# Performance work log

Measured on AMD Instinct MI355X. Metric: run time of the kernel, lower is better.

Reference implementation:

```python
import jax, jax.numpy as jnp
import numpy as np
from jax import lax

B, T, I, H = 32, 512, 512, 1024


def setup_inputs() -> dict:
    key = jax.random.key(0)
    k0, k1, k2, k3, k4 = jax.random.split(key, 5)
    s_i = 1.0 / np.sqrt(I).astype(np.float32)
    s_h = 1.0 / np.sqrt(H).astype(np.float32)
    x = jax.random.normal(k0, (B, T, I), dtype=jnp.float32)
    # stacked gate weights, order: input(i), forget(f), cell(g), output(o)
    Wx = jax.random.uniform(k1, (4 * H, I), jnp.float32, -s_i, s_i)
    bx = jax.random.uniform(k2, (4 * H,), jnp.float32, -s_i, s_i)
    Wh = jax.random.uniform(k3, (4 * H, H), jnp.float32, -s_h, s_h)
    bh = jax.random.uniform(k4, (4 * H,), jnp.float32, -s_h, s_h)
    return {"x": x, "Wx": Wx, "bx": bx, "Wh": Wh, "bh": bh}


def reference(x, Wx, bx, Wh, bh):
    # Pre-compute all input-to-gate projections in one batched GEMM: [B,T,4H]
    xg = jnp.einsum("bti,gi->btg", x, Wx) + bx + bh

    def step(carry, xg_t):
        h, c = carry
        gates = xg_t + h @ Wh.T  # [B,4H]
        i, f, g, o = jnp.split(gates, 4, axis=-1)
        i = jax.nn.sigmoid(i)
        f = jax.nn.sigmoid(f)
        g = jnp.tanh(g)
        o = jax.nn.sigmoid(o)
        c = f * c + i * g
        h = o * jnp.tanh(c)  # r is None in forward -> h_tilde = tanh(c)
        return (h, c), h

    b = x.shape[0]
    h0 = jnp.zeros((b, H), dtype=x.dtype)
    c0 = jnp.zeros((b, H), dtype=x.dtype)
    _, hs = lax.scan(step, (h0, c0), jnp.swapaxes(xg, 0, 1))  # hs: [T,B,H]
    return jnp.swapaxes(hs, 0, 1)  # [B,T,H]
```

## Files before the change

### kernel.cpp

```cpp
#include <hip/hip_runtime.h>
#include <hip/hip_bf16.h>

#define Bv 32
#define Tv 512
#define Iv 512
#define Hv 1024
#define NG 4096

typedef short bf16x8 __attribute__((ext_vector_type(8)));
typedef float floatx16 __attribute__((ext_vector_type(16)));
typedef unsigned short u16;
typedef unsigned long long u64;

__device__ __forceinline__ u16 f2bf(float f) {
  __hip_bfloat16 h = __float2bfloat16(f);
  return *reinterpret_cast<u16*>(&h);
}

__device__ __forceinline__ floatx16 mfma32(bf16x8 a, bf16x8 b, floatx16 c) {
  return __builtin_amdgcn_mfma_f32_32x32x16_bf16(a, b, c, 0, 0, 0);
}

__device__ __forceinline__ u64 ld_agent_u64(const u64* p) {
  return __hip_atomic_load(p, __ATOMIC_RELAXED, __HIP_MEMORY_SCOPE_AGENT);
}
__device__ __forceinline__ void st_agent_u16(u16* p, u16 v) {
  __hip_atomic_store(p, v, __ATOMIC_RELAXED, __HIP_MEMORY_SCOPE_AGENT);
}

__device__ __forceinline__ bf16x8 mk_frag(u64 lo, u64 hi) {
  union { u64 q[2]; bf16x8 v; } u;
  u.q[0] = lo; u.q[1] = hi;
  return u.v;
}

__global__ void k_init(unsigned int* p, int n) {
  int i = blockIdx.x * blockDim.x + threadIdx.x;
  if (i < n) p[i] = 0u;
}

__global__ void k_f2bf(const float* __restrict__ in, u16* __restrict__ out, int n) {
  int i = blockIdx.x * blockDim.x + threadIdx.x;
  if (i < n) out[i] = f2bf(in[i]);
}

__global__ void k_whf(const float* __restrict__ Wh, u16* __restrict__ whf) {
  int tid = blockIdx.x * 256 + threadIdx.x;
  int lane = tid & 63;
  int kt   = (tid >> 6) & 63;
  int nt   = (tid >> 12) & 1;
  int bl   = tid >> 13;
  int r    = nt * 32 + (lane & 31);
  int gate = r >> 4, du = r & 15;
  int row  = gate * Hv + bl * 16 + du;
  int k0   = kt * 16 + (lane >> 5) * 8;
  const float* s = Wh + (size_t)row * Hv + k0;
  u16* d = whf + (size_t)tid * 8;
#pragma unroll
  for (int j = 0; j < 8; ++j) d[j] = f2bf(s[j]);
}

__global__ __launch_bounds__(256) void k_xg(const u16* __restrict__ xb, const u16* __restrict__ wxb,
                                            const float* __restrict__ bx, const float* __restrict__ bh,
                                            float* __restrict__ xg, int t0, int tcshift) {
  __shared__ u16 Al[128 * 40];
  __shared__ u16 Bl[128 * 40];
  int tid = threadIdx.x;
  int wave = tid >> 6, lane = tid & 63;
  int wm = wave & 1, wn = wave >> 1;
  int bm = blockIdx.x, bn = blockIdx.y;
  int Tc = 1 << tcshift;

  floatx16 acc[2][2];
#pragma unroll
  for (int a = 0; a < 2; ++a)
#pragma unroll
    for (int c = 0; c < 2; ++c)
#pragma unroll
      for (int r = 0; r < 16; ++r) acc[a][c][r] = 0.f;

  int lr = tid >> 1;
  int lk = (tid & 1) * 16;
  int m  = bm * 128 + lr;
  int b  = m >> tcshift;
  int tl = m & (Tc - 1);
  const u16* asrc = xb + (size_t)(b * Tv + t0 + tl) * Iv + lk;
  int nrow = bn * 128 + lr;
  const u16* bsrc = wxb + (size_t)nrow * Iv + lk;
  u16* adst = &Al[lr * 40 + lk];
  u16* bdst = &Bl[lr * 40 + lk];

  for (int k0 = 0; k0 < Iv; k0 += 32) {
    __syncthreads();
    *(uint4*)adst       = *(const uint4*)(asrc);
    *(uint4*)(adst + 8) = *(const uint4*)(asrc + 8);
    *(uint4*)bdst       = *(const uint4*)(bsrc);
    *(uint4*)(bdst + 8) = *(const uint4*)(bsrc + 8);
    asrc += 32; bsrc += 32;
    __syncthreads();
#pragma unroll
    for (int kt = 0; kt < 2; ++kt) {
      int ko = kt * 16 + (lane >> 5) * 8;
      bf16x8 a0 = *(const bf16x8*)(&Al[(wm * 64 +      (lane & 31)) * 40 + ko]);
      bf16x8 a1 = *(const bf16x8*)(&Al[(wm * 64 + 32 + (lane & 31)) * 40 + ko]);
      bf16x8 b0 = *(const bf16x8*)(&Bl[(wn * 64 +      (lane & 31)) * 40 + ko]);
      bf16x8 b1 = *(const bf16x8*)(&Bl[(wn * 64 + 32 + (lane & 31)) * 40 + ko]);
      acc[0][0] = mfma32(a0, b0, acc[0][0]);
      acc[0][1] = mfma32(a0, b1, acc[0][1]);
      acc[1][0] = mfma32(a1, b0, acc[1][0]);
      acc[1][1] = mfma32(a1, b1, acc[1][1]);
    }
  }
#pragma unroll
  for (int mt = 0; mt < 2; ++mt) {
#pragma unroll
    for (int ntt = 0; ntt < 2; ++ntt) {
      int nGl = bn * 128 + wn * 64 + ntt * 32 + (lane & 31);
      float bias = bx[nGl] + bh[nGl];
#pragma unroll
      for (int r = 0; r < 16; ++r) {
        int mrow = (r & 3) + 8 * (r >> 2) + 4 * (lane >> 5);
        int mG = bm * 128 + wm * 64 + mt * 32 + mrow;
        int bb = mG >> tcshift;
        int tt = mG & (Tc - 1);
        xg[((size_t)(tt * Bv + bb) << 12) + nGl] = acc[mt][ntt][r] + bias;
      }
    }
  }
}

__global__ __launch_bounds__(256, 1) void k_scan(const u16* __restrict__ whf, const float* __restrict__ xg,
                                                 u64* __restrict__ hA, float* __restrict__ cbuf,
                                                 float* __restrict__ out, int* arrivals, int t0, int Tc) {
  __shared__ float red[2][4][64][36];
  __shared__ float obuf[16][2][16][16];
  int tid = threadIdx.x;
  int bl = blockIdx.x;
  int kh = tid >> 6, lane = tid & 63;
  int eu = tid & 15, eb = tid >> 4;
  int u0 = bl * 16;

  bf16x8 w0[16], w1[16];
  {
    const u16* wb0 = whf + ((size_t)(bl * 2 + 0) << 15);
    const u16* wb1 = whf + ((size_t)(bl * 2 + 1) << 15);
#pragma unroll
    for (int kk = 0; kk < 16; ++kk) {
      int kt = kh * 16 + kk;
      w0[kk] = *(const bf16x8*)(wb0 + (size_t)((kt << 6) + lane) * 8);
      w1[kk] = *(const bf16x8*)(wb1 + (size_t)((kt << 6) + lane) * 8);
    }
  }

  float c0, c1;
  if (t0 == 0) { c0 = 0.f; c1 = 0.f; }
  else {
    c0 = cbuf[eb * Hv + u0 + eu];
    c1 = cbuf[(eb + 16) * Hv + u0 + eu];
  }

  u16* hA16 = (u16*)hA;
  const int* fp = arrivals + ((kh << 4) + (lane & 15)) * 16;

  float xgv[4][2];
#pragma unroll
  for (int g = 0; g < 4; ++g)
#pragma unroll
    for (int b2 = 0; b2 < 2; ++b2)
      xgv[g][b2] = xg[((size_t)(0 * Bv + eb + 16 * b2) << 12) + g * Hv + u0 + eu];

  for (int tl = 0; tl < Tc; ++tl) {
    int t = t0 + tl;

    while (__hip_atomic_load(fp, __ATOMIC_RELAXED, __HIP_MEMORY_SCOPE_AGENT) < t) { }
    asm volatile("" ::: "memory");

    const u64* hAr = hA + (size_t)(t & 1) * 8192;

    u64 alo[16], ahi[16];
#pragma unroll
    for (int kk = 0; kk < 16; ++kk) {
      size_t fi = (size_t)((((kh << 4) + kk) << 6) + lane) * 2;
      alo[kk] = ld_agent_u64(hAr + fi);
      ahi[kk] = ld_agent_u64(hAr + fi + 1);
    }

    float xgn[4][2];
    {
      int tln = (tl + 1 < Tc) ? tl + 1 : tl;
#pragma unroll
      for (int g = 0; g < 4; ++g)
#pragma unroll
        for (int b2 = 0; b2 < 2; ++b2)
          xgn[g][b2] = xg[((size_t)(tln * Bv + eb + 16 * b2) << 12) + g * Hv + u0 + eu];
    }

    floatx16 acc0, acc1;
#pragma unroll
    for (int r = 0; r < 16; ++r) { acc0[r] = 0.f; acc1[r] = 0.f; }
#pragma unroll
    for (int kk = 0; kk < 16; ++kk) {
      bf16x8 a = mk_frag(alo[kk], ahi[kk]);
      acc0 = mfma32(a, w0[kk], acc0);
      acc1 = mfma32(a, w1[kk], acc1);
    }

    {
      int n = lane & 31;
      int bq = 4 * (lane >> 5);
#pragma unroll
      for (int rq = 0; rq < 4; ++rq) {
        float4 v0 = make_float4(acc0[rq * 4 + 0], acc0[rq * 4 + 1], acc0[rq * 4 + 2], acc0[rq * 4 + 3]);
        float4 v1 = make_float4(acc1[rq * 4 + 0], acc1[rq * 4 + 1], acc1[rq * 4 + 2], acc1[rq * 4 + 3]);
        *(float4*)&red[t & 1][kh][n][8 * rq + bq]      = v0;
        *(float4*)&red[t & 1][kh][32 + n][8 * rq + bq] = v1;
      }
    }

    __syncthreads();

    float hv0, hv1;
    {
      float gs[4][2];
#pragma unroll
      for (int g = 0; g < 4; ++g) {
        int r = g * 16 + eu;
#pragma unroll
        for (int b2 = 0; b2 < 2; ++b2) {
          int b = eb + 16 * b2;
          gs[g][b2] = red[t & 1][0][r][b] + red[t & 1][1][r][b] +
                      red[t & 1][2][r][b] + red[t & 1][3][r][b] + xgv[g][b2];
        }
      }
      float i0 = 1.f / (1.f + __expf(-gs[0][0]));
      float f0 = 1.f / (1.f + __expf(-gs[1][0]));
      float g0 = 1.f - 2.f / (__expf(2.f * gs[2][0]) + 1.f);
      float o0 = 1.f / (1.f + __expf(-gs[3][0]));
      c0 = f0 * c0 + i0 * g0;
      hv0 = o0 * (1.f - 2.f / (__expf(2.f * c0) + 1.f));

      float i1 = 1.f / (1.f + __expf(-gs[0][1]));
      float f1 = 1.f / (1.f + __expf(-gs[1][1]));
      float g1 = 1.f - 2.f / (__expf(2.f * gs[2][1]) + 1.f);
      float o1 = 1.f / (1.f + __expf(-gs[3][1]));
      c1 = f1 * c1 + i1 * g1;
      hv1 = o1 * (1.f - 2.f / (__expf(2.f * c1) + 1.f));
    }

    {
      int ts = tl & 15;
      obuf[ts][0][eb][eu] = hv0;
      obuf[ts][1][eb][eu] = hv1;
    }

    u16* hAw16 = hA16 + (size_t)((t + 1) & 1) * 32768;
    st_agent_u16(hAw16 + ((size_t)((bl << 6) + eb +      ((eu >> 3) << 5)) << 3) + (eu & 7), f2bf(hv0));
    st_agent_u16(hAw16 + ((size_t)((bl << 6) + eb + 16 + ((eu >> 3) << 5)) << 3) + (eu & 7), f2bf(hv1));
    asm volatile("s_waitcnt vmcnt(0)" ::: "memory");
    __syncthreads();

    if (tid == 0)
      __hip_atomic_store(arrivals + bl * 16, t + 1, __ATOMIC_RELAXED, __HIP_MEMORY_SCOPE_AGENT);

    if ((tl & 15) == 15 || tl == Tc - 1) {
      int ns = (tl & 15) + 1;
      int tb = t - (tl & 15);
      for (int ts = 0; ts < ns; ++ts) {
        out[((size_t)(eb * Tv + tb + ts) << 10) + u0 + eu]        = obuf[ts][0][eb][eu];
        out[((size_t)((eb + 16) * Tv + tb + ts) << 10) + u0 + eu] = obuf[ts][1][eb][eu];
      }
    }

#pragma unroll
    for (int g = 0; g < 4; ++g)
#pragma unroll
      for (int b2 = 0; b2 < 2; ++b2) xgv[g][b2] = xgn[g][b2];
  }
  cbuf[eb * Hv + u0 + eu] = c0;
  cbuf[(eb + 16) * Hv + u0 + eu] = c1;
}

extern "C" void kernel_launch(void* const* d_in, const int* in_sizes, int n_in,
                              void* d_out, int out_size, void* d_ws, size_t ws_size,
                              hipStream_t stream) {
  const float* x  = (const float*)d_in[0];
  const float* Wx = (const float*)d_in[1];
  const float* bx = (const float*)d_in[2];
  const float* Wh = (const float*)d_in[3];
  const float* bh = (const float*)d_in[4];
  float* out = (float*)d_out;
  char* ws = (char*)d_ws;

  int*   arrivals = (int*)ws;
  u64*   hA  = (u64*)(ws + 4096);
  float* cb  = (float*)(ws + 4096 + (128 << 10));
  u16*   xb  = (u16*)(ws + 4096 + (256 << 10));
  u16*   wxb = xb + (size_t)Bv * Tv * Iv;
  u16*   whf = wxb + (size_t)NG * Iv;
  float* xg  = (float*)(whf + (size_t)64 * 2 * 64 * 64 * 8);

  size_t fixedB = 4096 + (256ull << 10) +
                  ((size_t)Bv * Tv * Iv + (size_t)NG * Iv + (size_t)64 * 2 * 64 * 64 * 8) * 2;
  int tcshift = 9;
  while (tcshift > 2 && fixedB + (((size_t)Bv * NG * 4) << tcshift) > ws_size) --tcshift;
  int Tc = 1 << tcshift;

  k_init<<<132, 256, 0, stream>>>((unsigned int*)ws, (4096 + (128 << 10)) / 4);
  k_f2bf<<<(Bv * Tv * Iv) / 256, 256, 0, stream>>>(x, xb, Bv * Tv * Iv);
  k_f2bf<<<(NG * Iv) / 256, 256, 0, stream>>>(Wx, wxb, NG * Iv);
  k_whf<<<2048, 256, 0, stream>>>(Wh, whf);

  for (int t0 = 0; t0 < Tv; t0 += Tc) {
    k_xg<<<dim3(Tc / 4, 32), 256, 0, stream>>>(xb, wxb, bx, bh, xg, t0, tcshift);
    k_scan<<<64, 256, 0, stream>>>(whf, xg, hA, cb, out, arrivals, t0, Tc);
  }
}
```

Before: 2.391 ms.

## Replace arrival-counter barrier with timestep-tagged h values polled directly

Drops the per-block arrival counters and spin-wait. Each bf16 h value is now stored as a 32-bit word whose upper half carries the timestep tag, so consumers poll the h buffer itself with sc1 loads and retry until every tag matches the current step. This removes the store-drain, block barrier and flag publish from each step's critical path, and the MFMA work is consumed in four groups as they arrive. It doubles the h buffer size and adds perm/compare work. The LDS reduction buffer also gets an XOR swizzle to cut bank conflicts, and the xg prefetch is moved after the MFMA stage.

New measurement: 2.783 ms. +16.4%, slower.

```diff
diff --git a/kernel.cpp b/kernel.cpp
--- a/kernel.cpp
+++ b/kernel.cpp
@@ -10,7 +10,9 @@
 typedef short bf16x8 __attribute__((ext_vector_type(8)));
 typedef float floatx16 __attribute__((ext_vector_type(16)));
 typedef unsigned short u16;
+typedef unsigned int u32;
 typedef unsigned long long u64;
+typedef u32 u32x4 __attribute__((ext_vector_type(4)));
 
 __device__ __forceinline__ u16 f2bf(float f) {
   __hip_bfloat16 h = __float2bfloat16(f);
@@ -21,17 +23,18 @@
   return __builtin_amdgcn_mfma_f32_32x32x16_bf16(a, b, c, 0, 0, 0);
 }
 
-__device__ __forceinline__ u64 ld_agent_u64(const u64* p) {
-  return __hip_atomic_load(p, __ATOMIC_RELAXED, __HIP_MEMORY_SCOPE_AGENT);
-}
-__device__ __forceinline__ void st_agent_u16(u16* p, u16 v) {
+__device__ __forceinline__ void st_agent_u32(u32* p, u32 v) {
   __hip_atomic_store(p, v, __ATOMIC_RELAXED, __HIP_MEMORY_SCOPE_AGENT);
 }
 
-__device__ __forceinline__ bf16x8 mk_frag(u64 lo, u64 hi) {
-  union { u64 q[2]; bf16x8 v; } u;
-  u.q[0] = lo; u.q[1] = hi;
-  return u.v;
+__device__ __forceinline__ u32x4 ld16_sc1(const u32x4* p) {
+  u32x4 d;
+  asm volatile("global_load_dwordx4 %0, %1, off sc1" : "=v"(d) : "v"(p) : "memory");
+  return d;
+}
+
+__device__ __forceinline__ u32 permb(u32 a, u32 b, u32 sel) {
+  return __builtin_amdgcn_perm(a, b, sel);
 }
 
 __global__ void k_init(unsigned int* p, int n) {
@@ -130,8 +133,8 @@
 }
 
 __global__ __launch_bounds__(256, 1) void k_scan(const u16* __restrict__ whf, const float* __restrict__ xg,
-                                                 u64* __restrict__ hA, float* __restrict__ cbuf,
-                                                 float* __restrict__ out, int* arrivals, int t0, int Tc) {
+                                                 u32* __restrict__ hAv, float* __restrict__ cbuf,
+                                                 float* __restrict__ out, int t0, int Tc) {
   __shared__ float red[2][4][64][36];
   __shared__ float obuf[16][2][16][16];
   int tid = threadIdx.x;
@@ -159,9 +162,6 @@
     c1 = cbuf[(eb + 16) * Hv + u0 + eu];
   }
 
-  u16* hA16 = (u16*)hA;
-  const int* fp = arrivals + ((kh << 4) + (lane & 15)) * 16;
-
   float xgv[4][2];
 #pragma unroll
   for (int g = 0; g < 4; ++g)
@@ -171,50 +171,89 @@
 
   for (int tl = 0; tl < Tc; ++tl) {
     int t = t0 + tl;
-
-    while (__hip_atomic_load(fp, __ATOMIC_RELAXED, __HIP_MEMORY_SCOPE_AGENT) < t) { }
-    asm volatile("" ::: "memory");
-
-    const u64* hAr = hA + (size_t)(t & 1) * 8192;
-
-    u64 alo[16], ahi[16];
-#pragma unroll
-    for (int kk = 0; kk < 16; ++kk) {
-      size_t fi = (size_t)((((kh << 4) + kk) << 6) + lane) * 2;
-      alo[kk] = ld_agent_u64(hAr + fi);
-      ahi[kk] = ld_agent_u64(hAr + fi + 1);
-    }
-
-    float xgn[4][2];
-    {
-      int tln = (tl + 1 < Tc) ? tl + 1 : tl;
-#pragma unroll
-      for (int g = 0; g < 4; ++g)
-#pragma unroll
-        for (int b2 = 0; b2 < 2; ++b2)
-          xgn[g][b2] = xg[((size_t)(tln * Bv + eb + 16 * b2) << 12) + g * Hv + u0 + eu];
-    }
+    const u32x4* hr = (const u32x4*)(hAv + (size_t)(t & 1) * 32768);
+    u32 ee = ((u32)(t & 0xffff) << 16) | (u32)(t & 0xffff);
 
     floatx16 acc0, acc1;
 #pragma unroll
     for (int r = 0; r < 16; ++r) { acc0[r] = 0.f; acc1[r] = 0.f; }
-#pragma unroll
-    for (int kk = 0; kk < 16; ++kk) {
-      bf16x8 a = mk_frag(alo[kk], ahi[kk]);
-      acc0 = mfma32(a, w0[kk], acc0);
-      acc1 = mfma32(a, w1[kk], acc1);
+
+    u32x4 vb[4][8];
+#pragma unroll
+    for (int g = 0; g < 4; ++g) {
+#pragma unroll
+      for (int q = 0; q < 4; ++q) {
+        int kt = (kh << 4) + (g << 2) + q;
+        const u32x4* p = hr + (((size_t)((kt << 6) + lane)) << 1);
+        vb[g][2 * q]     = ld16_sc1(p);
+        vb[g][2 * q + 1] = ld16_sc1(p + 1);
+      }
+    }
+
+#pragma unroll
+    for (int g = 0; g < 4; ++g) {
+      if (g == 0)      asm volatile("s_waitcnt vmcnt(24)" ::: "memory");
+      else if (g == 1) asm volatile("s_waitcnt vmcnt(16)" ::: "memory");
+      else if (g == 2) asm volatile("s_waitcnt vmcnt(8)" ::: "memory");
+      else             asm volatile("s_waitcnt vmcnt(0)" ::: "memory");
+      __builtin_amdgcn_sched_barrier(0);
+
+      for (;;) {
+        int ok = 1;
+#pragma unroll
+        for (int i = 0; i < 8; ++i) {
+          u32x4 w = vb[g][i];
+          ok &= (permb(w.x, w.y, 0x03020706u) == ee);
+          ok &= (permb(w.z, w.w, 0x03020706u) == ee);
+        }
+        if (__all(ok)) break;
+#pragma unroll
+        for (int q = 0; q < 4; ++q) {
+          int kt = (kh << 4) + (g << 2) + q;
+          const u32x4* p = hr + (((size_t)((kt << 6) + lane)) << 1);
+          vb[g][2 * q]     = ld16_sc1(p);
+          vb[g][2 * q + 1] = ld16_sc1(p + 1);
+        }
+        asm volatile("s_waitcnt vmcnt(0)" ::: "memory");
+        __builtin_amdgcn_sched_barrier(0);
+      }
+
+#pragma unroll
+      for (int q = 0; q < 4; ++q) {
+        u32x4 lo = vb[g][2 * q], hi2 = vb[g][2 * q + 1];
+        u32x4 f;
+        f.x = permb(lo.x,  lo.y,  0x01000504u);
+        f.y = permb(lo.z,  lo.w,  0x01000504u);
+        f.z = permb(hi2.x, hi2.y, 0x01000504u);
+        f.w = permb(hi2.z, hi2.w, 0x01000504u);
+        union { u32x4 u; bf16x8 b; } cv; cv.u = f;
+        int kk = (g << 2) + q;
+        acc0 = mfma32(cv.b, w0[kk], acc0);
+        acc1 = mfma32(cv.b, w1[kk], acc1);
+      }
     }
 
     {
       int n = lane & 31;
       int bq = 4 * (lane >> 5);
+      int key = ((n >> 3) & 3) << 2;
 #pragma unroll
       for (int rq = 0; rq < 4; ++rq) {
         float4 v0 = make_float4(acc0[rq * 4 + 0], acc0[rq * 4 + 1], acc0[rq * 4 + 2], acc0[rq * 4 + 3]);
         float4 v1 = make_float4(acc1[rq * 4 + 0], acc1[rq * 4 + 1], acc1[rq * 4 + 2], acc1[rq * 4 + 3]);
-        *(float4*)&red[t & 1][kh][n][8 * rq + bq]      = v0;
-        *(float4*)&red[t & 1][kh][32 + n][8 * rq + bq] = v1;
-      }
+        *(float4*)&red[t & 1][kh][n][(8 * rq + bq) ^ key]      = v0;
+        *(float4*)&red[t & 1][kh][32 + n][(8 * rq + bq) ^ key] = v1;
+      }
+    }
+
+    float xgn[4][2];
+    {
+      int tln = (tl + 1 < Tc) ? tl + 1 : tl;
+#pragma unroll
+      for (int g = 0; g < 4; ++g)
+#pragma unroll
+        for (int b2 = 0; b2 < 2; ++b2)
+          xgn[g][b2] = xg[((size_t)(tln * Bv + eb + 16 * b2) << 12) + g * Hv + u0 + eu];
     }
 
     __syncthreads();
@@ -225,9 +264,10 @@
 #pragma unroll
       for (int g = 0; g < 4; ++g) {
         int r = g * 16 + eu;
+        int keyr = ((r >> 3) & 3) << 2;
 #pragma unroll
         for (int b2 = 0; b2 < 2; ++b2) {
-          int b = eb + 16 * b2;
+          int b = (eb + 16 * b2) ^ keyr;
           gs[g][b2] = red[t & 1][0][r][b] + red[t & 1][1][r][b] +
                       red[t & 1][2][r][b] + red[t & 1][3][r][b] + xgv[g][b2];
         }
@@ -253,14 +293,12 @@
       obuf[ts][1][eb][eu] = hv1;
     }
 
-    u16* hAw16 = hA16 + (size_t)((t + 1) & 1) * 32768;
-    st_agent_u16(hAw16 + ((size_t)((bl << 6) + eb +      ((eu >> 3) << 5)) << 3) + (eu & 7), f2bf(hv0));
-    st_agent_u16(hAw16 + ((size_t)((bl << 6) + eb + 16 + ((eu >> 3) << 5)) << 3) + (eu & 7), f2bf(hv1));
-    asm volatile("s_waitcnt vmcnt(0)" ::: "memory");
-    __syncthreads();
-
-    if (tid == 0)
-      __hip_atomic_store(arrivals + bl * 16, t + 1, __ATOMIC_RELAXED, __HIP_MEMORY_SCOPE_AGENT);
+    {
+      u32* hw = hAv + (size_t)((t + 1) & 1) * 32768;
+      u32 tg = ((u32)((t + 1) & 0xffff)) << 16;
+      st_agent_u32(hw + (((size_t)((bl << 6) + eb +      ((eu >> 3) << 5)) << 3) + (eu & 7)), tg | (u32)f2bf(hv0));
+      st_agent_u32(hw + (((size_t)((bl << 6) + eb + 16 + ((eu >> 3) << 5)) << 3) + (eu & 7)), tg | (u32)f2bf(hv1));
+    }
 
     if ((tl & 15) == 15 || tl == Tc - 1) {
       int ns = (tl & 15) + 1;
@@ -291,27 +329,26 @@
   float* out = (float*)d_out;
   char* ws = (char*)d_ws;
 
-  int*   arrivals = (int*)ws;
-  u64*   hA  = (u64*)(ws + 4096);
-  float* cb  = (float*)(ws + 4096 + (128 << 10));
-  u16*   xb  = (u16*)(ws + 4096 + (256 << 10));
+  u32*   hAv = (u32*)(ws + 4096);
+  float* cb  = (float*)(ws + 4096 + (256 << 10));
+  u16*   xb  = (u16*)(ws + 4096 + (384 << 10));
   u16*   wxb = xb + (size_t)Bv * Tv * Iv;
   u16*   whf = wxb + (size_t)NG * Iv;
   float* xg  = (float*)(whf + (size_t)64 * 2 * 64 * 64 * 8);
 
-  size_t fixedB = 4096 + (256ull << 10) +
+  size_t fixedB = 4096 + (384ull << 10) +
                   ((size_t)Bv * Tv * Iv + (size_t)NG * Iv + (size_t)64 * 2 * 64 * 64 * 8) * 2;
   int tcshift = 9;
   while (tcshift > 2 && fixedB + (((size_t)Bv * NG * 4) << tcshift) > ws_size) --tcshift;
   int Tc = 1 << tcshift;
 
-  k_init<<<132, 256, 0, stream>>>((unsigned int*)ws, (4096 + (128 << 10)) / 4);
+  k_init<<<260, 256, 0, stream>>>((unsigned int*)ws, (4096 + (256 << 10)) / 4);
   k_f2bf<<<(Bv * Tv * Iv) / 256, 256, 0, stream>>>(x, xb, Bv * Tv * Iv);
   k_f2bf<<<(NG * Iv) / 256, 256, 0, stream>>>(Wx, wxb, NG * Iv);
   k_whf<<<2048, 256, 0, stream>>>(Wh, whf);
 
   for (int t0 = 0; t0 < Tv; t0 += Tc) {
     k_xg<<<dim3(Tc / 4, 32), 256, 0, stream>>>(xb, wxb, bx, bh, xg, t0, tcshift);
-    k_scan<<<64, 256, 0, stream>>>(whf, xg, hA, cb, out, arrivals, t0, Tc);
-  }
-}
+    k_scan<<<64, 256, 0, stream>>>(whf, xg, hAv, cb, out, t0, Tc);
+  }
+}
```
